# Kernel optimization log

Measured on AMD Instinct MI355X. Metric: run time of the kernel, lower is better.

The kernel has to match this reference:

```python
import jax, jax.numpy as jnp
import numpy as np

B, T, N = 512, 1024, 50
ROOT_IDX, END_IDX = 0, 1
NEG_INF = -10000.0


def setup_inputs() -> dict:
    key = jax.random.key(0)
    k1, k2, k3, k4 = jax.random.split(key, 4)
    input_features = jax.random.normal(k1, (B, T, N), dtype=jnp.float32)
    # xavier_uniform on [N, N]: bound = sqrt(6 / (N + N))
    bound = float(np.sqrt(6.0 / (N + N)))
    log_transitions = jax.random.uniform(k2, (N, N), minval=-bound, maxval=bound, dtype=jnp.float32)
    log_transitions = log_transitions.at[:, ROOT_IDX].set(NEG_INF)
    log_transitions = log_transitions.at[END_IDX, :].set(NEG_INF)
    target_tags = jax.random.randint(k3, (B, T), 0, N).astype(jnp.int64)
    # contiguous prefix mask from random lengths in [T//2, T]
    lengths = jax.random.randint(k4, (B,), T // 2, T + 1)
    input_mask = (jnp.arange(T)[None, :] < lengths[:, None]).astype(jnp.int32)
    return {
        "input_features": input_features,
        "log_transitions": log_transitions,
        "target_tags": target_tags,
        "input_mask": input_mask,
    }


def _crf_nll(input_features, log_transitions, target_tags, input_mask):
    maskf = input_mask.astype(input_features.dtype)  # [B, T]

    # ---- forward belief propagation (log partition) ----
    alpha0 = log_transitions[ROOT_IDX, :][None, :] + input_features[:, 0, :]  # [B, N]
    feats_t = jnp.swapaxes(input_features, 0, 1)  # [T, B, N]
    mask_t = jnp.swapaxes(maskf, 0, 1)            # [T, B]

    def step(alpha, xs):
        feat, m = xs  # [B, N], [B]
        # next_tag_var[b, i, j] = alpha[b, i] + feat[b, j] + trans[i, j]
        nxt = alpha[:, :, None] + feat[:, None, :] + log_transitions[None, :, :]
        new = jax.nn.logsumexp(nxt, axis=1)  # [B, N]
        m = m[:, None]
        return new * m + alpha * (1.0 - m), None

    alpha, _ = jax.lax.scan(step, alpha0, (feats_t[1:], mask_t[1:]))
    log_z = jax.nn.logsumexp(alpha + log_transitions[:, END_IDX][None, :], axis=-1)  # [B]

    # ---- gold sequence score (vectorized over time) ----
    tags = target_tags  # [B, T]
    scores = log_transitions[ROOT_IDX, tags[:, 0]]  # [B]
    # per-position emission score of the gold tag
    emis = jnp.take_along_axis(input_features, tags[:, :, None], axis=2)[:, :, 0]  # [B, T]
    trans = log_transitions[tags[:, :-1], tags[:, 1:]]  # [B, T-1]
    scores = scores + jnp.sum(trans * maskf[:, 1:], axis=1) + jnp.sum(emis[:, :-1] * maskf[:, :-1], axis=1)
    last_idx = jnp.sum(input_mask, axis=1) - 1  # [B]
    last_tags = jnp.take_along_axis(tags, last_idx[:, None], axis=1)[:, 0]  # [B]
    last_emit = jnp.take_along_axis(input_features[:, -1, :], last_tags[:, None], axis=1)[:, 0]
    scores = scores + log_transitions[last_tags, END_IDX] + last_emit * maskf[:, -1]

    return log_z - scores  # negative log likelihood, [B]


def reference(input_features, log_transitions, target_tags, input_mask):
    return _crf_nll(input_features, log_transitions, target_tags, input_mask)
```

## Files before the change

### kernel.cpp

```cpp
#include <hip/hip_runtime.h>
#include <math.h>

#define BB 512
#define TT 1024
#define NS 50

typedef _Float16 half2_t __attribute__((ext_vector_type(2)));

static __device__ __forceinline__ half2_t pk_h2(float a, float b) {
    auto r = __builtin_amdgcn_cvt_pkrtz(a, b);
    return __builtin_bit_cast(half2_t, r);
}
static __device__ __forceinline__ float wave_max_f(float v) {
    #pragma unroll
    for (int k = 32; k >= 1; k >>= 1) v = fmaxf(v, __shfl_xor(v, k, 64));
    return v;
}
static __device__ __forceinline__ float wave_sum_f(float v) {
    #pragma unroll
    for (int k = 32; k >= 1; k >>= 1) v += __shfl_xor(v, k, 64);
    return v;
}
static __device__ __forceinline__ int wave_sum_i(int v) {
    #pragma unroll
    for (int k = 32; k >= 1; k >>= 1) v += __shfl_xor(v, k, 64);
    return v;
}
static __device__ __forceinline__ half2_t bcast_h2(half2_t v, int lane) {
    int u = __builtin_amdgcn_readlane(__builtin_bit_cast(int, v), lane);
    return __builtin_bit_cast(half2_t, u);
}

__global__ __launch_bounds__(128, 1) void crf_nll_kernel(
    const float* __restrict__ feat,
    const float* __restrict__ trans,
    const int*   __restrict__ tags,
    const int*   __restrict__ mask,
    float* __restrict__ out)
{
    const int b    = blockIdx.x;
    const int tid  = threadIdx.x;
    const int w    = tid >> 6;
    const int lane = tid & 63;
    const int jj   = (lane < NS) ? lane : 0;

    __shared__ float sh_comb[64];
    __shared__ float sh_sc[2];

#define INIT_E(m) half2_t e##m; { \
        int r0 = w ? (jj * NS + 2*(m)) : ((2*(m)) * NS + jj); \
        int r1 = r0 + (w ? 1 : NS); \
        float x0 = __expf(trans[r0]); \
        float x1 = __expf(trans[r1]); \
        if (lane >= NS) { x0 = 0.0f; x1 = 0.0f; } \
        e##m = pk_h2(x0, x1); }
    INIT_E(0)  INIT_E(1)  INIT_E(2)  INIT_E(3)  INIT_E(4)
    INIT_E(5)  INIT_E(6)  INIT_E(7)  INIT_E(8)  INIT_E(9)
    INIT_E(10) INIT_E(11) INIT_E(12) INIT_E(13) INIT_E(14)
    INIT_E(15) INIT_E(16) INIT_E(17) INIT_E(18) INIT_E(19)
    INIT_E(20) INIT_E(21) INIT_E(22) INIT_E(23) INIT_E(24)
#undef INIT_E

    int cnt = 0;
    for (int t = lane; t < TT; t += 64) cnt += mask[b * TT + t];
    const int len = wave_sum_i(cnt);
    const int tm  = (len - 1) >> 1;
    const int nst = w ? (len - 1 - tm) : tm;

    const float* fb = feat + (size_t)b * TT * NS;

    float v;
    if (w == 0) v = (lane < NS) ? (trans[jj] + fb[jj]) : -INFINITY;
    else        v = (lane < NS) ? (trans[jj * NS + 1] + fb[(size_t)(len - 1) * NS + jj])
                                : -INFINITY;
    float off = wave_max_f(v);

    auto step = [&](float f) {
        float p = __expf(v - off);
        int pn = __builtin_amdgcn_update_dpp(
            __float_as_int(p), __float_as_int(p), 0xB1, 0xF, 0xF, true);
        half2_t pp = pk_h2(p, __int_as_float(pn));
#define RL(m) half2_t r##m = bcast_h2(pp, 2*(m));
        RL(0)  RL(1)  RL(2)  RL(3)  RL(4)  RL(5)  RL(6)  RL(7)
        RL(8)  RL(9)  RL(10) RL(11) RL(12) RL(13) RL(14) RL(15)
        RL(16) RL(17) RL(18) RL(19) RL(20) RL(21) RL(22) RL(23) RL(24)
#undef RL
        __builtin_amdgcn_sched_barrier(0);
#define DOT(acc, m) acc = __builtin_amdgcn_fdot2(r##m, e##m, acc, false)
        float s0 = 0.f, s1 = 0.f, s2 = 0.f, s3 = 0.f;
        float s4 = 0.f, s5 = 0.f, s6 = 0.f, s7 = 0.f;
        DOT(s0, 0);  DOT(s1, 1);  DOT(s2, 2);  DOT(s3, 3);
        DOT(s4, 4);  DOT(s5, 5);  DOT(s6, 6);  DOT(s7, 7);
        DOT(s0, 8);  DOT(s1, 9);  DOT(s2, 10); DOT(s3, 11);
        DOT(s4, 12); DOT(s5, 13); DOT(s6, 14); DOT(s7, 15);
        DOT(s0, 16); DOT(s1, 17); DOT(s2, 18); DOT(s3, 19);
        DOT(s4, 20); DOT(s5, 21); DOT(s6, 22); DOT(s7, 23);
        DOT(s0, 24);
#undef DOT
        float s = ((s0 + s1) + (s2 + s3)) + ((s4 + s5) + (s6 + s7));
        v = f + off + __logf(s);
        off = __int_as_float(__builtin_amdgcn_readlane(__float_as_int(v), 7)) + 2.0f;
    };

    float q0, q1, q2, q3, q4, q5, q6, q7;
    {
        int t0 = w ? (len - 2) : 1;
        int st = w ? -1 : 1;
#define LD(qr, d) { int tl = t0 + st * (d); tl = (tl < 0) ? 0 : ((tl < TT) ? tl : TT - 1); \
                    qr = fb[(size_t)tl * NS + jj]; }
        LD(q0, 0) LD(q1, 1) LD(q2, 2) LD(q3, 3) LD(q4, 4) LD(q5, 5) LD(q6, 6) LD(q7, 7)
#undef LD
    }

#define PF_STEP(qr, d) { \
        float f = qr; \
        int kl = k + 8 + (d); \
        int tl = w ? (len - 2 - kl) : (1 + kl); \
        tl = (tl < 0) ? 0 : ((tl < TT) ? tl : TT - 1); \
        qr = fb[(size_t)tl * NS + jj]; \
        step(f); }

    int k = 0;
    for (; k + 8 <= nst; k += 8) {
        PF_STEP(q0, 0) PF_STEP(q1, 1) PF_STEP(q2, 2) PF_STEP(q3, 3)
        PF_STEP(q4, 4) PF_STEP(q5, 5) PF_STEP(q6, 6) PF_STEP(q7, 7)
    }
#undef PF_STEP
    for (; k < nst; ++k) {
        int tl = w ? (len - 2 - k) : (1 + k);
        step(fb[(size_t)tl * NS + jj]);
    }

    if (w == 1) {
        sh_comb[lane] = v - fb[(size_t)tm * NS + jj];
    }

    const int* tb = tags + (size_t)b * TT;
    float sc = 0.0f;
    for (int t2 = tid; t2 < len; t2 += 128) {
        int tg = tb[t2];
        sc += fb[(size_t)t2 * NS + tg];
        if (t2 >= 1) sc += trans[tb[t2 - 1] * NS + tg];
    }
    sc = wave_sum_f(sc);
    if (lane == 0) sh_sc[w] = sc;

    __syncthreads();

    if (w == 0) {
        float z = v + sh_comb[lane];
        float M = wave_max_f(z);
        float Z = wave_sum_f(__expf(z - M));
        float log_z = M + __logf(Z);
        if (lane == 0) {
            float sct = sh_sc[0] + sh_sc[1]
                      + trans[tb[0]]
                      + trans[tb[len - 1] * NS + 1];
            out[b] = log_z - sct;
        }
    }
}

extern "C" void kernel_launch(void* const* d_in, const int* in_sizes, int n_in,
                              void* d_out, int out_size, void* d_ws, size_t ws_size,
                              hipStream_t stream) {
    const float* feat  = (const float*)d_in[0];
    const float* trans = (const float*)d_in[1];
    const int*   tags  = (const int*)d_in[2];
    const int*   mask  = (const int*)d_in[3];
    float* out = (float*)d_out;
    crf_nll_kernel<<<dim3(BB), dim3(128), 0, stream>>>(feat, trans, tags, mask, out);
}
```

Baseline: 301.8 us.

## Run CRF forward recursion in linear space with exponent rescaling and LDS broadcast

```diff
diff --git a/kernel.cpp b/kernel.cpp
--- a/kernel.cpp
+++ b/kernel.cpp
@@ -11,11 +11,6 @@
     auto r = __builtin_amdgcn_cvt_pkrtz(a, b);
     return __builtin_bit_cast(half2_t, r);
 }
-static __device__ __forceinline__ float wave_max_f(float v) {
-    #pragma unroll
-    for (int k = 32; k >= 1; k >>= 1) v = fmaxf(v, __shfl_xor(v, k, 64));
-    return v;
-}
 static __device__ __forceinline__ float wave_sum_f(float v) {
     #pragma unroll
     for (int k = 32; k >= 1; k >>= 1) v += __shfl_xor(v, k, 64);
@@ -26,10 +21,8 @@
     for (int k = 32; k >= 1; k >>= 1) v += __shfl_xor(v, k, 64);
     return v;
 }
-static __device__ __forceinline__ half2_t bcast_h2(half2_t v, int lane) {
-    int u = __builtin_amdgcn_readlane(__builtin_bit_cast(int, v), lane);
-    return __builtin_bit_cast(half2_t, u);
-}
+#define FDOT(a, b, c) __builtin_amdgcn_fdot2((a), (b), (c), false)
+#define H2(x) __builtin_bit_cast(half2_t, x)
 
 __global__ __launch_bounds__(128, 1) void crf_nll_kernel(
     const float* __restrict__ feat,
@@ -44,15 +37,19 @@
     const int lane = tid & 63;
     const int jj   = (lane < NS) ? lane : 0;
 
+    __shared__ __align__(16) float sbuf[2][32];
     __shared__ float sh_comb[64];
     __shared__ float sh_sc[2];
+    __shared__ int   sh_Kb;
+
+    float* mybuf = &sbuf[w][0];
 
 #define INIT_E(m) half2_t e##m; { \
         int r0 = w ? (jj * NS + 2*(m)) : ((2*(m)) * NS + jj); \
         int r1 = r0 + (w ? 1 : NS); \
         float x0 = __expf(trans[r0]); \
         float x1 = __expf(trans[r1]); \
-        if (lane >= NS) { x0 = 0.0f; x1 = 0.0f; } \
+        if (lane >= NS) { x0 = 0.f; x1 = 0.f; } \
         e##m = pk_h2(x0, x1); }
     INIT_E(0)  INIT_E(1)  INIT_E(2)  INIT_E(3)  INIT_E(4)
     INIT_E(5)  INIT_E(6)  INIT_E(7)  INIT_E(8)  INIT_E(9)
@@ -69,37 +66,48 @@
 
     const float* fb = feat + (size_t)b * TT * NS;
 
-    float v;
-    if (w == 0) v = (lane < NS) ? (trans[jj] + fb[jj]) : -INFINITY;
-    else        v = (lane < NS) ? (trans[jj * NS + 1] + fb[(size_t)(len - 1) * NS + jj])
-                                : -INFINITY;
-    float off = wave_max_f(v);
+    float u;
+    if (w == 0) u = (lane < NS) ? __expf(trans[jj] + fb[jj]) : 0.f;
+    else        u = (lane < NS) ? __expf(trans[jj * NS + 1] + fb[(size_t)(len - 1) * NS + jj]) : 0.f;
+    int K = 0, kp, rr;
+    { int bb2 = __builtin_amdgcn_readlane(__float_as_int(u), 7);
+      kp = ((bb2 >> 23) & 255) - 127; rr = (127 - kp) << 23; }
 
-    auto step = [&](float f) {
-        float p = __expf(v - off);
-        int pn = __builtin_amdgcn_update_dpp(
+    auto step = [&](float eexp) {
+        K += kp;
+        float p = u * __int_as_float(rr);
+        int pn_ = __builtin_amdgcn_update_dpp(
             __float_as_int(p), __float_as_int(p), 0xB1, 0xF, 0xF, true);
-        half2_t pp = pk_h2(p, __int_as_float(pn));
-#define RL(m) half2_t r##m = bcast_h2(pp, 2*(m));
-        RL(0)  RL(1)  RL(2)  RL(3)  RL(4)  RL(5)  RL(6)  RL(7)
-        RL(8)  RL(9)  RL(10) RL(11) RL(12) RL(13) RL(14) RL(15)
-        RL(16) RL(17) RL(18) RL(19) RL(20) RL(21) RL(22) RL(23) RL(24)
-#undef RL
-        __builtin_amdgcn_sched_barrier(0);
-#define DOT(acc, m) acc = __builtin_amdgcn_fdot2(r##m, e##m, acc, false)
+        float pnf = __int_as_float(pn_);
+        bool od = (lane & 1);
+        float lo = od ? pnf : p;
+        float hi = od ? p : pnf;
+        half2_t pk = pk_h2(lo, hi);
+        mybuf[lane >> 1] = __builtin_bit_cast(float, pk);
+        __asm__ volatile("s_waitcnt lgkmcnt(0)" ::: "memory");
+        const float4* m4 = (const float4*)mybuf;
+        float4 c0 = m4[0], c1 = m4[1], c2 = m4[2], c3 = m4[3];
+        float4 c4 = m4[4], c5 = m4[5], c6 = m4[6];
         float s0 = 0.f, s1 = 0.f, s2 = 0.f, s3 = 0.f;
         float s4 = 0.f, s5 = 0.f, s6 = 0.f, s7 = 0.f;
-        DOT(s0, 0);  DOT(s1, 1);  DOT(s2, 2);  DOT(s3, 3);
-        DOT(s4, 4);  DOT(s5, 5);  DOT(s6, 6);  DOT(s7, 7);
-        DOT(s0, 8);  DOT(s1, 9);  DOT(s2, 10); DOT(s3, 11);
-        DOT(s4, 12); DOT(s5, 13); DOT(s6, 14); DOT(s7, 15);
-        DOT(s0, 16); DOT(s1, 17); DOT(s2, 18); DOT(s3, 19);
-        DOT(s4, 20); DOT(s5, 21); DOT(s6, 22); DOT(s7, 23);
-        DOT(s0, 24);
-#undef DOT
-        float s = ((s0 + s1) + (s2 + s3)) + ((s4 + s5) + (s6 + s7));
-        v = f + off + __logf(s);
-        off = __int_as_float(__builtin_amdgcn_readlane(__float_as_int(v), 7)) + 2.0f;
+        s0 = FDOT(H2(c0.x), e0,  s0); s1 = FDOT(H2(c0.y), e1,  s1);
+        s2 = FDOT(H2(c0.z), e2,  s2); s3 = FDOT(H2(c0.w), e3,  s3);
+        s4 = FDOT(H2(c1.x), e4,  s4); s5 = FDOT(H2(c1.y), e5,  s5);
+        s6 = FDOT(H2(c1.z), e6,  s6); s7 = FDOT(H2(c1.w), e7,  s7);
+        s0 = FDOT(H2(c2.x), e8,  s0); s1 = FDOT(H2(c2.y), e9,  s1);
+        s2 = FDOT(H2(c2.z), e10, s2); s3 = FDOT(H2(c2.w), e11, s3);
+        s4 = FDOT(H2(c3.x), e12, s4); s5 = FDOT(H2(c3.y), e13, s5);
+        s6 = FDOT(H2(c3.z), e14, s6); s7 = FDOT(H2(c3.w), e15, s7);
+        s0 = FDOT(H2(c4.x), e16, s0); s1 = FDOT(H2(c4.y), e17, s1);
+        s2 = FDOT(H2(c4.z), e18, s2); s3 = FDOT(H2(c4.w), e19, s3);
+        s4 = FDOT(H2(c5.x), e20, s4); s5 = FDOT(H2(c5.y), e21, s5);
+        s6 = FDOT(H2(c5.z), e22, s6); s7 = FDOT(H2(c5.w), e23, s7);
+        s0 = FDOT(H2(c6.x), e24, s0);
+        float S = ((s0 + s1) + (s2 + s3)) + ((s4 + s5) + (s6 + s7));
+        u = S * eexp;
+        int bb2 = __builtin_amdgcn_readlane(__float_as_int(u), 7);
+        kp = ((bb2 >> 23) & 255) - 127;
+        rr = (127 - kp) << 23;
     };
 
     float q0, q1, q2, q3, q4, q5, q6, q7;
@@ -107,18 +115,18 @@
         int t0 = w ? (len - 2) : 1;
         int st = w ? -1 : 1;
 #define LD(qr, d) { int tl = t0 + st * (d); tl = (tl < 0) ? 0 : ((tl < TT) ? tl : TT - 1); \
-                    qr = fb[(size_t)tl * NS + jj]; }
+                    qr = __expf(fb[(size_t)tl * NS + jj]); }
         LD(q0, 0) LD(q1, 1) LD(q2, 2) LD(q3, 3) LD(q4, 4) LD(q5, 5) LD(q6, 6) LD(q7, 7)
 #undef LD
     }
 
 #define PF_STEP(qr, d) { \
-        float f = qr; \
+        float e_ = qr; \
         int kl = k + 8 + (d); \
         int tl = w ? (len - 2 - kl) : (1 + kl); \
         tl = (tl < 0) ? 0 : ((tl < TT) ? tl : TT - 1); \
-        qr = fb[(size_t)tl * NS + jj]; \
-        step(f); }
+        qr = __expf(fb[(size_t)tl * NS + jj]); \
+        step(e_); }
 
     int k = 0;
     for (; k + 8 <= nst; k += 8) {
@@ -128,11 +136,12 @@
 #undef PF_STEP
     for (; k < nst; ++k) {
         int tl = w ? (len - 2 - k) : (1 + k);
-        step(fb[(size_t)tl * NS + jj]);
+        step(__expf(fb[(size_t)tl * NS + jj]));
     }
 
     if (w == 1) {
-        sh_comb[lane] = v - fb[(size_t)tm * NS + jj];
+        sh_comb[lane] = u * __expf(-fb[(size_t)tm * NS + jj]);
+        if (lane == 0) sh_Kb = K;
     }
 
     const int* tb = tags + (size_t)b * TT;
@@ -148,10 +157,9 @@
     __syncthreads();
 
     if (w == 0) {
-        float z = v + sh_comb[lane];
-        float M = wave_max_f(z);
-        float Z = wave_sum_f(__expf(z - M));
-        float log_z = M + __logf(Z);
+        float wv = u * sh_comb[lane];
+        float W = wave_sum_f(wv);
+        float log_z = __logf(W) + (float)(K + sh_Kb) * 0.6931471805599453f;
         if (lane == 0) {
             float sct = sh_sc[0] + sh_sc[1]
                       + trans[tb[0]]
```

Result: faster. 268.1 us (-11.2%).
